# Kernel optimization log

Measured on AMD Instinct MI355X. Metric: run time of the kernel, lower is better.

## Reference

```python
import jax, jax.numpy as jnp
import numpy as np

B, T, C, E, K = 8, 2048, 1024, 8, 2
CAP = int(T / E * 1.25)  # expert capacity per batch row = 320


def setup_inputs() -> dict:
    key = jax.random.key(0)
    ks = jax.random.split(key, 6)
    s = lambda k, shape, fan: jax.random.normal(k, shape, jnp.float32) / np.sqrt(fan)
    return dict(
        x=jax.random.normal(ks[0], (B, T, C), jnp.float32),
        rw1=s(ks[1], (C, 4 * C), C), rb1=jnp.zeros((4 * C,), jnp.float32),
        rw2=s(ks[2], (4 * C, 4 * C), 4 * C), rb2=jnp.zeros((4 * C,), jnp.float32),
        rw3=s(ks[3], (4 * C, E), 4 * C), rb3=jnp.zeros((E,), jnp.float32),
        ew1=s(ks[4], (E, C, 4 * C), C), eb1=jnp.zeros((E, 4 * C), jnp.float32),
        ew2=s(ks[5], (E, 4 * C, C), 4 * C), eb2=jnp.zeros((E, C), jnp.float32),
    )


def reference(x, rw1, rb1, rw2, rb2, rw3, rb3, ew1, eb1, ew2, eb2):
    # Router (dropout is identity in eval): MLP -> softmax over experts
    h = jax.nn.relu(x @ rw1 + rb1)
    h = jax.nn.relu(h @ rw2 + rb2)
    probs = jax.nn.softmax(h @ rw3 + rb3, axis=-1)        # [B,T,E]
    topk_p, topk_e = jax.lax.top_k(probs, K)              # [B,T,K]

    b_ids = jnp.broadcast_to(jnp.arange(B)[:, None], (B, T))
    out = jnp.zeros_like(x)
    # Loop over small fixed number of experts (mirrors per-rank expert compute)
    for e in range(E):
        sel = (topk_e == e)                               # [B,T,K]
        mask = sel.any(-1)                                # token routed to expert e
        gate = (topk_p * sel).sum(-1)                     # unnormalized top-k prob
        pos = jnp.cumsum(mask, axis=1) - 1                # slot within capacity buffer
        keep = mask & (pos < CAP)                         # capacity truncation (drop overflow)
        pos_s = jnp.where(keep, pos, CAP)                 # CAP is out-of-range -> dropped
        # Dispatch: scatter kept tokens into [B, CAP, C] capacity-padded buffer
        buf = jnp.zeros((B, CAP, C), x.dtype).at[b_ids, pos_s].set(x, mode='drop')
        # Expert FFN on padded buffer
        y = jax.nn.relu(buf @ ew1[e] + eb1[e]) @ ew2[e] + eb2[e]
        # Combine: gather back to token positions, weight by gate
        g = y[b_ids, jnp.where(keep, pos, 0)]
        out = out + gate[..., None] * jnp.where(keep[..., None], g, jnp.zeros((), x.dtype))
    return out
```

## Files before the change

kernel.cpp:

```cpp
#include <hip/hip_runtime.h>
#include <stdint.h>

typedef _Float16 f16;
typedef _Float16 half8 __attribute__((ext_vector_type(8)));
typedef float f32x4 __attribute__((ext_vector_type(4)));

#define NF_MAX 2048
#define THETA  0.02f

__device__ __forceinline__ void gload16(const void* g, void* l) {
  __builtin_amdgcn_global_load_lds(
      (const __attribute__((address_space(1))) void*)g,
      (__attribute__((address_space(3))) void*)l, 16, 0, 0);
}

#define BAR() do { __builtin_amdgcn_s_barrier(); __builtin_amdgcn_sched_barrier(0); } while (0)
#define WAIT_VM8() do { asm volatile("s_waitcnt vmcnt(8)" ::: "memory"); __builtin_amdgcn_sched_barrier(0); } while (0)
#define WAIT_VM0() do { asm volatile("s_waitcnt vmcnt(0)" ::: "memory"); __builtin_amdgcn_sched_barrier(0); } while (0)

template<int EPI, bool SPLIT3>
__launch_bounds__(512, 2)
__global__ void gemm256(const f16* __restrict__ A0, const f16* __restrict__ A1,
                        const f16* __restrict__ B0, const f16* __restrict__ B1,
                        int N, int Kd, int lda, int ldb,
                        const int* __restrict__ rowsrcA, const f16* __restrict__ zeroPage,
                        const float* __restrict__ bias, int bias_stride, int rows_per_exp,
                        f16* __restrict__ oH, int ldo, float* __restrict__ oAcc,
                        const float* __restrict__ w3, float* __restrict__ oLog,
                        const int* __restrict__ nfp)
{
  __shared__ f16 lds[4 * 8192 * 2 + 512];
  f16* sA = lds;
  f16* sB = lds + 4 * 8192;
  f16* sDummy = lds + 8 * 8192;

  const int tid  = threadIdx.x;
  const int lane = tid & 63, w = tid >> 6;
  const int wm = w >> 2, wn = w & 3;

  const int gx  = gridDim.x;
  const int nwg = gx * gridDim.y;
  const int bid = blockIdx.y * gx + blockIdx.x;
  const int swz = (bid & 7) * (nwg >> 3) + (bid >> 3);
  const int by  = swz / gx, bx = swz - by * gx;
  const int m0  = by * 256, n0 = bx * 256;
  const int k0  = blockIdx.z * Kd;

  if (nfp) {
    int nf = *nfp; nf = nf < NF_MAX ? nf : NF_MAX;
    const int lim = (nf + 255) & ~255;
    if (m0 >= lim) return;
  }

  int e = 0;
  if (rows_per_exp > 0) e = m0 / rows_per_exp;
  const f16* Bh = B0 + (size_t)e * N * ldb;

  const int nk  = Kd >> 6;
  const int NIT = SPLIT3 ? 3 * nk : nk;

  const int sr  = lane & 15;
  const int sk8 = lane >> 4;

  size_t aoff[2], boff[2];
  bool az[2] = { false, false };
  #pragma unroll
  for (int jj = 0; jj < 2; ++jj) {
    const int arow = m0 + (jj * 8 + w) * 16 + sr;
    if (rowsrcA) {
      const int rs = rowsrcA[arow];
      az[jj] = (rs < 0);
      aoff[jj] = az[jj] ? 0 : (size_t)rs * lda;
    } else {
      aoff[jj] = (size_t)arow * lda;
    }
    boff[jj] = (size_t)(n0 + (jj * 8 + w) * 16 + sr) * ldb;
  }

  auto stageA = [&](const f16* base, int kk, int kc, f16* slotBase, bool valid) {
    #pragma unroll
    for (int jj = 0; jj < 2; ++jj) {
      const int mt = jj * 8 + w;
      f16* dst = valid ? (slotBase + mt * 512) : sDummy;
      const f16* src = az[jj] ? zeroPage
                              : base + aoff[jj] + (k0 + kk + kc * 32 + sk8 * 8);
      gload16(src, dst);
    }
  };
  auto stageB = [&](const f16* base, int kk, int kc, f16* slotBase, bool valid) {
    #pragma unroll
    for (int jj = 0; jj < 2; ++jj) {
      const int mt = jj * 8 + w;
      f16* dst = valid ? (slotBase + mt * 512) : sDummy;
      const f16* src = base + boff[jj] + (k0 + kk + kc * 32 + sk8 * 8);
      gload16(src, dst);
    }
  };

  struct It { const f16* Ab; const f16* Bb; int kk, kin, pass; };
  const f16* Ab0 = SPLIT3 ? A1 : A0;
  auto advance = [&](It& s) {
    if (s.kin + 1 < nk) { s.kin++; }
    else if (SPLIT3 && s.pass < 2) {
      s.kin = 0; s.pass++;
      s.Ab = (s.pass == 0) ? A1 : A0;
      s.Bb = (s.pass == 1) ? B1 : Bh;
    }
    s.kk = s.kin << 6;
  };
  It it1 = { Ab0, Bh, 64, 1, 0 };
  It it2 = { Ab0, Bh, 128, 2, 0 };

  stageA(Ab0, 0, 0, &sA[0], true);
  stageB(Bh,  0, 0, &sB[0], true);
  stageA(Ab0, 0, 1, &sA[8192], true);
  stageB(Bh,  0, 1, &sB[8192], true);
  stageA(it1.Ab, it1.kk, 0, &sA[2 * 8192], true);
  stageB(it1.Bb, it1.kk, 0, &sB[2 * 8192], true);
  WAIT_VM8();
  BAR();

  f32x4 acc[8][4] = {};
  const int aBase = wm * 8;
  const int bBase = wn * 4;

  auto mfma32 = [&](half8* a8, half8* bf) {
    __builtin_amdgcn_s_setprio(1);
    #pragma unroll
    for (int mi = 0; mi < 8; ++mi)
      #pragma unroll
      for (int ni = 0; ni < 4; ++ni)
        acc[mi][ni] = __builtin_amdgcn_mfma_f32_16x16x32_f16(
            a8[mi], bf[ni], acc[mi][ni], 0, 0, 0);
    __builtin_amdgcn_s_setprio(0);
  };
  auto rdA = [&](half8* dst, int slot, int mtb) {
    #pragma unroll
    for (int mi = 0; mi < 4; ++mi)
      dst[mi] = *(const half8*)&sA[slot * 8192 + (mtb + mi) * 512 + lane * 8];
  };
  auto rdB = [&](half8* dst, int slot) {
    #pragma unroll
    for (int ni = 0; ni < 4; ++ni)
      dst[ni] = *(const half8*)&sB[slot * 8192 + (bBase + ni) * 512 + lane * 8];
  };

  for (int t = 0; t < NIT; ++t) {
    const int sa0 = (2 * t) & 3, sa1 = sa0 ^ 1;
    const bool v1 = (t + 1 < NIT), v2 = (t + 2 < NIT);

    if (SPLIT3 && t == 2 * nk) {
      #pragma unroll
      for (int mi = 0; mi < 8; ++mi)
        #pragma unroll
        for (int ni = 0; ni < 4; ++ni)
          acc[mi][ni] = acc[mi][ni] * 2.44140625e-4f;
    }

    half8 a8[8], bF[4];

    rdA(&a8[0], sa0, aBase);
    rdA(&a8[4], sa0, aBase + 4);
    rdB(bF, sa0);
    stageA(it1.Ab, it1.kk, 1, &sA[(sa0 ^ 3) * 8192], v1);
    stageB(it1.Bb, it1.kk, 1, &sB[(sa0 ^ 3) * 8192], v1);
    WAIT_VM8();
    BAR();
    mfma32(a8, bF);
    BAR();

    rdA(&a8[0], sa1, aBase);
    rdA(&a8[4], sa1, aBase + 4);
    rdB(bF, sa1);
    stageA(it2.Ab, it2.kk, 0, &sA[sa0 * 8192], v2);
    stageB(it2.Bb, it2.kk, 0, &sB[sa0 * 8192], v2);
    WAIT_VM8();
    BAR();
    mfma32(a8, bF);
    BAR();

    it1 = it2;
    advance(it2);
  }
  WAIT_VM0();

  float bv[4] = { 0.f, 0.f, 0.f, 0.f };
  if (bias) {
    #pragma unroll
    for (int ni = 0; ni < 4; ++ni) {
      const int col = n0 + wn * 64 + ni * 16 + (lane & 15);
      bv[ni] = bias[(size_t)e * bias_stride + col];
    }
  }

  if (EPI == 2) {
    f32x4 wlo[4], whi[4];
    #pragma unroll
    for (int ni = 0; ni < 4; ++ni) {
      const int col = n0 + wn * 64 + ni * 16 + (lane & 15);
      wlo[ni] = *(const f32x4*)(w3 + (size_t)col * 8);
      whi[ni] = *(const f32x4*)(w3 + (size_t)col * 8 + 4);
    }
    const int p = (n0 >> 8) * 4 + wn;
    #pragma unroll
    for (int mi = 0; mi < 8; ++mi) {
      #pragma unroll
      for (int r = 0; r < 4; ++r) {
        const int row = m0 + wm * 128 + mi * 16 + (lane >> 4) * 4 + r;
        f32x4 plo = {}, phi = {};
        #pragma unroll
        for (int ni = 0; ni < 4; ++ni) {
          const float v = fmaxf(acc[mi][ni][r] + bv[ni], 0.f);
          plo += v * wlo[ni];
          phi += v * whi[ni];
        }
        #pragma unroll
        for (int msk = 1; msk < 16; msk <<= 1) {
          #pragma unroll
          for (int q = 0; q < 4; ++q) {
            plo[q] += __shfl_xor(plo[q], msk);
            phi[q] += __shfl_xor(phi[q], msk);
          }
        }
        if ((lane & 15) == 0) {
          float* dst = oLog + ((size_t)p * ldo + row) * 8;
          *(f32x4*)dst = plo;
          *(f32x4*)(dst + 4) = phi;
        }
      }
    }
  } else {
    #pragma unroll
    for (int mi = 0; mi < 8; ++mi) {
      #pragma unroll
      for (int r = 0; r < 4; ++r) {
        const int row = m0 + wm * 128 + mi * 16 + (lane >> 4) * 4 + r;
        #pragma unroll
        for (int ni = 0; ni < 4; ++ni) {
          const int col = n0 + wn * 64 + ni * 16 + (lane & 15);
          if (EPI == 3) {
            atomicAdd(&oAcc[(size_t)row * ldo + col], acc[mi][ni][r]);
          } else {
            float v = acc[mi][ni][r] + bv[ni];
            if (EPI == 0) v = fmaxf(v, 0.f);
            oH[(size_t)row * ldo + col] = (f16)v;
          }
        }
      }
    }
  }
}

__global__ void split_x(const float* __restrict__ x, f16* __restrict__ hi,
                        f16* __restrict__ lo, int n)
{
  const int i = blockIdx.x * 256 + threadIdx.x;
  if (i * 8 >= n) return;
  const f32x4 a = ((const f32x4*)x)[2 * i];
  const f32x4 b = ((const f32x4*)x)[2 * i + 1];
  half8 h, l;
  #pragma unroll
  for (int j = 0; j < 4; ++j) {
    float v = a[j]; f16 hh = (f16)v;
    h[j] = hh; l[j] = (f16)((v - (float)hh) * 4096.0f);
    v = b[j]; hh = (f16)v;
    h[4 + j] = hh; l[4 + j] = (f16)((v - (float)hh) * 4096.0f);
  }
  ((half8*)hi)[i] = h;
  ((half8*)lo)[i] = l;
}

template<bool SPLIT>
__global__ void transpose_conv(const float* __restrict__ in, f16* __restrict__ oh,
                               f16* __restrict__ ol, int R, int Cc)
{
  __shared__ float tile[64][65];
  const size_t boff = (size_t)blockIdx.z * R * Cc;
  in += boff; oh += boff;
  if (SPLIT) ol += boff;
  const int c0 = blockIdx.x * 64, r0 = blockIdx.y * 64;
  #pragma unroll
  for (int i = 0; i < 16; ++i) {
    const int idx = i * 256 + threadIdx.x;
    const int r = idx >> 6, c = idx & 63;
    tile[r][c] = in[(size_t)(r0 + r) * Cc + (c0 + c)];
  }
  __syncthreads();
  #pragma unroll
  for (int i = 0; i < 16; ++i) {
    const int idx = i * 256 + threadIdx.x;
    const int ro = idx >> 6, co = idx & 63;
    const float v = tile[co][ro];
    const f16 h = (f16)v;
    const size_t o = (size_t)(c0 + ro) * R + (r0 + co);
    oh[o] = h;
    if (SPLIT) ol[o] = (f16)((v - (float)h) * 4096.0f);
  }
}

__global__ void topk_flag(const float* __restrict__ part, const float* __restrict__ b3,
                          int* __restrict__ eidx, float* __restrict__ gval,
                          int* __restrict__ flags, int* __restrict__ nfc)
{
  const int t = blockIdx.x * 256 + threadIdx.x;
  float l[8];
  #pragma unroll
  for (int e = 0; e < 8; ++e) l[e] = b3[e];
  for (int p = 0; p < 64; ++p) {
    const float* src = part + ((size_t)p * 16384 + t) * 8;
    const f32x4 a = *(const f32x4*)src;
    const f32x4 b = *(const f32x4*)(src + 4);
    #pragma unroll
    for (int q = 0; q < 4; ++q) { l[q] += a[q]; l[4 + q] += b[q]; }
  }
  float mx = l[0];
  #pragma unroll
  for (int e = 1; e < 8; ++e) mx = fmaxf(mx, l[e]);
  float ex[8], s = 0.f;
  #pragma unroll
  for (int e = 0; e < 8; ++e) { ex[e] = expf(l[e] - mx); s += ex[e]; }
  float p1 = -1.f, p2 = -1.f; int e1 = 0, e2 = 0;
  #pragma unroll
  for (int e = 0; e < 8; ++e) {
    const float pe = ex[e] / s;
    if (pe > p1)      { p2 = p1; e2 = e1; p1 = pe; e1 = e; }
    else if (pe > p2) { p2 = pe; e2 = e; }
  }
  eidx[t * 2] = e1; eidx[t * 2 + 1] = e2;
  gval[t * 2] = p1; gval[t * 2 + 1] = p2;
  float l1 = -1e30f, l2 = -1e30f, l3 = -1e30f;
  #pragma unroll
  for (int e = 0; e < 8; ++e) {
    const float le = l[e];
    if (le > l1)      { l3 = l2; l2 = l1; l1 = le; }
    else if (le > l2) { l3 = l2; l2 = le; }
    else if (le > l3) { l3 = le; }
  }
  if (l2 - l3 < THETA) {
    const int s0 = atomicAdd(nfc, 1);
    if (s0 < NF_MAX) flags[s0] = t;
  }
}

__global__ void post1(const float* __restrict__ h1r, const float* __restrict__ b1,
                      f16* __restrict__ hh, f16* __restrict__ hl,
                      const int* __restrict__ nfc)
{
  int nf = *nfc; nf = nf < NF_MAX ? nf : NF_MAX;
  const int lim = (nf + 255) & ~255;
  const int row = blockIdx.x;
  if (row >= lim) return;
  const int j = blockIdx.y * 2048 + threadIdx.x * 8;
  const float* src = h1r + (size_t)row * 4096 + j;
  const f32x4 a = *(const f32x4*)src;
  const f32x4 b = *(const f32x4*)(src + 4);
  half8 h, l;
  #pragma unroll
  for (int k = 0; k < 4; ++k) {
    float v = fmaxf(a[k] + b1[j + k], 0.f);
    f16 x = (f16)v; h[k] = x; l[k] = (f16)((v - (float)x) * 4096.0f);
    v = fmaxf(b[k] + b1[j + 4 + k], 0.f);
    x = (f16)v; h[4 + k] = x; l[4 + k] = (f16)((v - (float)x) * 4096.0f);
  }
  *(half8*)(hh + (size_t)row * 4096 + j) = h;
  *(half8*)(hl + (size_t)row * 4096 + j) = l;
}

__global__ void logits_exact(const float* __restrict__ h2r, const float* __restrict__ b2,
                             const float* __restrict__ w3, const float* __restrict__ b3,
                             const int* __restrict__ flags, const int* __restrict__ nfc,
                             int* __restrict__ eidx, float* __restrict__ gval)
{
  const int srow = blockIdx.x;
  int nf = *nfc; nf = nf < NF_MAX ? nf : NF_MAX;
  if (srow >= nf) return;
  const float* hrow = h2r + (size_t)srow * 4096;
  double p[8];
  #pragma unroll
  for (int e = 0; e < 8; ++e) p[e] = 0.0;
  for (int i = 0; i < 16; ++i) {
    const int k = i * 256 + threadIdx.x;
    const double h = (double)fmaxf(hrow[k] + b2[k], 0.f);
    const float* wp = w3 + (size_t)k * 8;
    #pragma unroll
    for (int e = 0; e < 8; ++e) p[e] += h * (double)wp[e];
  }
  #pragma unroll
  for (int e = 0; e < 8; ++e)
    for (int off = 32; off > 0; off >>= 1)
      p[e] += __shfl_down(p[e], off);
  __shared__ double sp[4][8];
  const int lane = threadIdx.x & 63, wv = threadIdx.x >> 6;
  if (lane == 0) {
    #pragma unroll
    for (int e = 0; e < 8; ++e) sp[wv][e] = p[e];
  }
  __syncthreads();
  if (threadIdx.x == 0) {
    float l[8];
    #pragma unroll
    for (int e = 0; e < 8; ++e)
      l[e] = (float)(sp[0][e] + sp[1][e] + sp[2][e] + sp[3][e] + (double)b3[e]);
    float mx = l[0];
    for (int e = 1; e < 8; ++e) mx = fmaxf(mx, l[e]);
    float ex[8], s = 0.f;
    for (int e = 0; e < 8; ++e) { ex[e] = expf(l[e] - mx); s += ex[e]; }
    float p1 = -1.f, p2 = -1.f; int e1 = 0, e2 = 0;
    for (int e = 0; e < 8; ++e) {
      const float pe = ex[e] / s;
      if (pe > p1)      { p2 = p1; e2 = e1; p1 = pe; e1 = e; }
      else if (pe > p2) { p2 = pe; e2 = e; }
    }
    const int tok = flags[srow];
    eidx[tok * 2] = e1; eidx[tok * 2 + 1] = e2;
    gval[tok * 2] = p1; gval[tok * 2 + 1] = p2;
  }
}

__global__ void route_scan(const int* __restrict__ eidx, const float* __restrict__ gval,
                           int* __restrict__ cnt, int* __restrict__ rowsrc,
                           int* __restrict__ tokslot)
{
  const int pair = blockIdx.x;
  const int e = pair >> 3, b = pair & 7;
  const int lane = threadIdx.x;
  int running = 0;
  for (int t0 = 0; t0 < 2048; t0 += 64) {
    const int t = t0 + lane;
    const int i2 = (b * 2048 + t) * 2;
    const int m0 = (eidx[i2] == e), m1 = (eidx[i2 + 1] == e);
    const int m = m0 | m1;
    const unsigned long long bal = __ballot(m);
    const int pos = running + __popcll(bal & ((1ull << lane) - 1ull));
    if (m && pos < 320) {
      const int slot = pair * 320 + pos;
      rowsrc[slot] = b * 2048 + t;
      tokslot[(b * 2048 + t) * 2 + (m0 ? 0 : 1)] = slot;
    }
    running += __popcll(bal);
  }
  const int c = running < 320 ? running : 320;
  for (int s = c + lane; s < 320; s += 64) rowsrc[pair * 320 + s] = -1;
  if (lane == 0) cnt[pair] = c;
}

__global__ void combine(const f16* __restrict__ yb, const int* __restrict__ tokslot,
                        const float* __restrict__ gval, float* __restrict__ out)
{
  const int t = blockIdx.x;
  const int s0 = tokslot[t * 2], s1 = tokslot[t * 2 + 1];
  const float g0 = gval[t * 2], g1 = gval[t * 2 + 1];
  float a[8] = {};
  if (s0 >= 0) {
    const half8 y = ((const half8*)(yb + (size_t)s0 * 1024))[threadIdx.x];
    #pragma unroll
    for (int k = 0; k < 8; ++k) a[k] += g0 * (float)y[k];
  }
  if (s1 >= 0) {
    const half8 y = ((const half8*)(yb + (size_t)s1 * 1024))[threadIdx.x];
    #pragma unroll
    for (int k = 0; k < 8; ++k) a[k] += g1 * (float)y[k];
  }
  float* dst = out + (size_t)t * 1024 + threadIdx.x * 8;
  f32x4 lo = { a[0], a[1], a[2], a[3] }, hi = { a[4], a[5], a[6], a[7] };
  *(f32x4*)dst = lo;
  *(f32x4*)(dst + 4) = hi;
}

extern "C" void kernel_launch(void* const* d_in, const int* in_sizes, int n_in,
                              void* d_out, int out_size, void* d_ws, size_t ws_size,
                              hipStream_t stream)
{
  (void)in_sizes; (void)n_in; (void)out_size;
  const float* x   = (const float*)d_in[0];
  const float* rw1 = (const float*)d_in[1];
  const float* rb1 = (const float*)d_in[2];
  const float* rw2 = (const float*)d_in[3];
  const float* rb2 = (const float*)d_in[4];
  const float* rw3 = (const float*)d_in[5];
  const float* rb3 = (const float*)d_in[6];
  const float* ew1 = (const float*)d_in[7];
  const float* eb1 = (const float*)d_in[8];
  const float* ew2 = (const float*)d_in[9];
  const float* eb2 = (const float*)d_in[10];

  constexpr size_t MB = 1024ull * 1024ull;
  constexpr size_t KB = 1024ull;
  char* ws = (char*)d_ws;
  if (ws_size < 401 * MB) return;

  f16*   h1f  = (f16*)(ws);
  f16*   ew1t = (f16*)(ws);
  f16*   ew2t = (f16*)(ws + 64 * MB);
  f16*   xhi  = (f16*)(ws + 128 * MB);
  char*  S    = ws + 160 * MB;
  int*   eidx   = (int*)(S);
  float* gval   = (float*)(S + 128 * KB);
  int*   cnt    = (int*)(S + 256 * KB);
  int*   nfc    = (int*)(S + 260 * KB);
  int*   flags  = (int*)(S + 264 * KB);
  int*   tokslot= (int*)(S + 272 * KB);
  int*   rowsrc = (int*)(S + 400 * KB);
  f16*   zeros  = (f16*)(S + 480 * KB);
  f16*   xlo    = (f16*)(ws + 161 * MB);
  f16*   rw1thi = (f16*)(ws + 193 * MB);
  f16*   rw1tlo = (f16*)(ws + 201 * MB);
  f16*   rw2thi = (f16*)(ws + 209 * MB);
  f16*   rw2tlo = (f16*)(ws + 241 * MB);
  float* part   = (float*)(ws + 273 * MB);
  float* h1r    = (float*)(ws + 305 * MB);
  float* h2r    = (float*)(ws + 337 * MB);
  f16*   h1rh   = (f16*)(ws + 369 * MB);
  f16*   h1rl   = (f16*)(ws + 385 * MB);
  f16*   h_e    = (f16*)(ws + 161 * MB);
  f16*   yb     = (f16*)(ws + 321 * MB);

  hipMemsetAsync(nfc, 0, 4, stream);
  hipMemsetAsync(tokslot, 0xFF, 128 * KB, stream);
  hipMemsetAsync(zeros, 0, 16 * KB, stream);
  hipMemsetAsync(h1r, 0, 64 * MB, stream);

  split_x<<<8192, 256, 0, stream>>>(x, xhi, xlo, 16384 * 1024);
  transpose_conv<true ><<<dim3(64, 16, 1), 256, 0, stream>>>(rw1, rw1thi, rw1tlo, 1024, 4096);
  transpose_conv<true ><<<dim3(64, 64, 1), 256, 0, stream>>>(rw2, rw2thi, rw2tlo, 4096, 4096);

  gemm256<0, false><<<dim3(16, 64), 512, 0, stream>>>(
      xhi, nullptr, rw1thi, nullptr, 4096, 1024, 1024, 1024,
      nullptr, nullptr, rb1, 0, 0,
      h1f, 4096, nullptr, nullptr, nullptr, nullptr);
  gemm256<2, false><<<dim3(16, 64), 512, 0, stream>>>(
      h1f, nullptr, rw2thi, nullptr, 4096, 4096, 4096, 4096,
      nullptr, nullptr, rb2, 0, 0,
      nullptr, 16384, nullptr, rw3, part, nullptr);
  topk_flag<<<64, 256, 0, stream>>>(part, rb3, eidx, gval, flags, nfc);

  gemm256<3, true><<<dim3(16, 8, 2), 512, 0, stream>>>(
      xhi, xlo, rw1thi, rw1tlo, 4096, 512, 1024, 1024,
      flags, zeros, nullptr, 0, 0,
      nullptr, 4096, h1r, nullptr, nullptr, nfc);
  post1<<<dim3(2048, 2), 256, 0, stream>>>(h1r, rb1, h1rh, h1rl, nfc);
  gemm256<3, true><<<dim3(16, 8, 4), 512, 0, stream>>>(
      h1rh, h1rl, rw2thi, rw2tlo, 4096, 1024, 4096, 4096,
      nullptr, nullptr, nullptr, 0, 0,
      nullptr, 4096, h2r, nullptr, nullptr, nfc);
  logits_exact<<<NF_MAX, 256, 0, stream>>>(h2r, rb2, rw3, rb3, flags, nfc,
                                           eidx, gval);

  route_scan<<<64, 64, 0, stream>>>(eidx, gval, cnt, rowsrc, tokslot);

  transpose_conv<false><<<dim3(64, 16, 8), 256, 0, stream>>>(ew1, ew1t, nullptr, 1024, 4096);
  transpose_conv<false><<<dim3(16, 64, 8), 256, 0, stream>>>(ew2, ew2t, nullptr, 4096, 1024);

  gemm256<0, false><<<dim3(16, 80), 512, 0, stream>>>(
      xhi, nullptr, ew1t, nullptr, 4096, 1024, 1024, 1024,
      rowsrc, zeros, eb1, 4096, 2560,
      h_e, 4096, nullptr, nullptr, nullptr, nullptr);
  gemm256<1, false><<<dim3(4, 80), 512, 0, stream>>>(
      h_e, nullptr, ew2t, nullptr, 1024, 4096, 4096, 4096,
      nullptr, nullptr, eb2, 1024, 2560,
      yb, 1024, nullptr, nullptr, nullptr, nullptr);

  combine<<<16384, 128, 0, stream>>>(yb, tokslot, gval, (float*)d_out);
}
```

Before: 1.821 ms.

## Replace pipelined 256x256 GEMM with simpler single-buffered 128x128 tile GEMM

Swaps the 512-thread, 256x256-tile GEMM, which used a multi-slot LDS ring with vmcnt-based prefetch, for a 256-thread 128x128-tile kernel. The new kernel loads one K=32 chunk per iteration and brackets it with __syncthreads. The aim is more workgroups, higher occupancy and less LDS and register pressure per block. In exchange it loses the global-to-LDS prefetch overlap and halves per-tile data reuse, so the GEMMs may become more latency- and bandwidth-bound.

```diff
diff --git a/kernel.cpp b/kernel.cpp
--- a/kernel.cpp
+++ b/kernel.cpp
@@ -14,13 +14,9 @@
       (__attribute__((address_space(3))) void*)l, 16, 0, 0);
 }
 
-#define BAR() do { __builtin_amdgcn_s_barrier(); __builtin_amdgcn_sched_barrier(0); } while (0)
-#define WAIT_VM8() do { asm volatile("s_waitcnt vmcnt(8)" ::: "memory"); __builtin_amdgcn_sched_barrier(0); } while (0)
-#define WAIT_VM0() do { asm volatile("s_waitcnt vmcnt(0)" ::: "memory"); __builtin_amdgcn_sched_barrier(0); } while (0)
-
 template<int EPI, bool SPLIT3>
-__launch_bounds__(512, 2)
-__global__ void gemm256(const f16* __restrict__ A0, const f16* __restrict__ A1,
+__launch_bounds__(256, 4)
+__global__ void gemm128(const f16* __restrict__ A0, const f16* __restrict__ A1,
                         const f16* __restrict__ B0, const f16* __restrict__ B1,
                         int N, int Kd, int lda, int ldb,
                         const int* __restrict__ rowsrcA, const f16* __restrict__ zeroPage,
@@ -29,26 +25,23 @@
                         const float* __restrict__ w3, float* __restrict__ oLog,
                         const int* __restrict__ nfp)
 {
-  __shared__ f16 lds[4 * 8192 * 2 + 512];
-  f16* sA = lds;
-  f16* sB = lds + 4 * 8192;
-  f16* sDummy = lds + 8 * 8192;
-
-  const int tid  = threadIdx.x;
-  const int lane = tid & 63, w = tid >> 6;
-  const int wm = w >> 2, wn = w & 3;
+  __shared__ f16 sA[4096];
+  __shared__ f16 sB[4096];
+
+  const int lane = threadIdx.x & 63, w = threadIdx.x >> 6;
+  const int wm = w >> 1, wn = w & 1;
 
   const int gx  = gridDim.x;
   const int nwg = gx * gridDim.y;
   const int bid = blockIdx.y * gx + blockIdx.x;
   const int swz = (bid & 7) * (nwg >> 3) + (bid >> 3);
   const int by  = swz / gx, bx = swz - by * gx;
-  const int m0  = by * 256, n0 = bx * 256;
+  const int m0  = by * 128, n0 = bx * 128;
   const int k0  = blockIdx.z * Kd;
 
   if (nfp) {
     int nf = *nfp; nf = nf < NF_MAX ? nf : NF_MAX;
-    const int lim = (nf + 255) & ~255;
+    const int lim = (nf + 127) & ~127;
     if (m0 >= lim) return;
   }
 
@@ -56,7 +49,7 @@
   if (rows_per_exp > 0) e = m0 / rows_per_exp;
   const f16* Bh = B0 + (size_t)e * N * ldb;
 
-  const int nk  = Kd >> 6;
+  const int nk  = Kd >> 5;
   const int NIT = SPLIT3 ? 3 * nk : nk;
 
   const int sr  = lane & 15;
@@ -66,7 +59,7 @@
   bool az[2] = { false, false };
   #pragma unroll
   for (int jj = 0; jj < 2; ++jj) {
-    const int arow = m0 + (jj * 8 + w) * 16 + sr;
+    const int arow = m0 + (jj * 4 + w) * 16 + sr;
     if (rowsrcA) {
       const int rs = rowsrcA[arow];
       az[jj] = (rs < 0);
@@ -74,115 +67,53 @@
     } else {
       aoff[jj] = (size_t)arow * lda;
     }
-    boff[jj] = (size_t)(n0 + (jj * 8 + w) * 16 + sr) * ldb;
-  }
-
-  auto stageA = [&](const f16* base, int kk, int kc, f16* slotBase, bool valid) {
+    boff[jj] = (size_t)(n0 + (jj * 4 + w) * 16 + sr) * ldb;
+  }
+
+  f32x4 acc[4][4] = {};
+  int kin = 0, pass = 0;
+
+  for (int t = 0; t < NIT; ++t) {
+    const f16* Ab;
+    const f16* Bb;
+    if (SPLIT3) {
+      if (t == 2 * nk) {
+        #pragma unroll
+        for (int mi = 0; mi < 4; ++mi)
+          #pragma unroll
+          for (int ni = 0; ni < 4; ++ni)
+            acc[mi][ni] = acc[mi][ni] * 2.44140625e-4f;
+      }
+      Ab = (pass == 0) ? A1 : A0;
+      Bb = (pass == 1) ? B1 : Bh;
+    } else { Ab = A0; Bb = Bh; }
+    const int kk = k0 + (kin << 5) + sk8 * 8;
+
     #pragma unroll
     for (int jj = 0; jj < 2; ++jj) {
-      const int mt = jj * 8 + w;
-      f16* dst = valid ? (slotBase + mt * 512) : sDummy;
-      const f16* src = az[jj] ? zeroPage
-                              : base + aoff[jj] + (k0 + kk + kc * 32 + sk8 * 8);
-      gload16(src, dst);
-    }
-  };
-  auto stageB = [&](const f16* base, int kk, int kc, f16* slotBase, bool valid) {
-    #pragma unroll
-    for (int jj = 0; jj < 2; ++jj) {
-      const int mt = jj * 8 + w;
-      f16* dst = valid ? (slotBase + mt * 512) : sDummy;
-      const f16* src = base + boff[jj] + (k0 + kk + kc * 32 + sk8 * 8);
-      gload16(src, dst);
-    }
-  };
-
-  struct It { const f16* Ab; const f16* Bb; int kk, kin, pass; };
-  const f16* Ab0 = SPLIT3 ? A1 : A0;
-  auto advance = [&](It& s) {
-    if (s.kin + 1 < nk) { s.kin++; }
-    else if (SPLIT3 && s.pass < 2) {
-      s.kin = 0; s.pass++;
-      s.Ab = (s.pass == 0) ? A1 : A0;
-      s.Bb = (s.pass == 1) ? B1 : Bh;
-    }
-    s.kk = s.kin << 6;
-  };
-  It it1 = { Ab0, Bh, 64, 1, 0 };
-  It it2 = { Ab0, Bh, 128, 2, 0 };
-
-  stageA(Ab0, 0, 0, &sA[0], true);
-  stageB(Bh,  0, 0, &sB[0], true);
-  stageA(Ab0, 0, 1, &sA[8192], true);
-  stageB(Bh,  0, 1, &sB[8192], true);
-  stageA(it1.Ab, it1.kk, 0, &sA[2 * 8192], true);
-  stageB(it1.Bb, it1.kk, 0, &sB[2 * 8192], true);
-  WAIT_VM8();
-  BAR();
-
-  f32x4 acc[8][4] = {};
-  const int aBase = wm * 8;
-  const int bBase = wn * 4;
-
-  auto mfma32 = [&](half8* a8, half8* bf) {
-    __builtin_amdgcn_s_setprio(1);
-    #pragma unroll
-    for (int mi = 0; mi < 8; ++mi)
+      const int ch = jj * 4 + w;
+      gload16(az[jj] ? zeroPage : (Ab + aoff[jj] + kk), (void*)&sA[ch * 512]);
+      gload16(Bb + boff[jj] + kk,                       (void*)&sB[ch * 512]);
+    }
+    __syncthreads();
+
+    half8 aF[4], bF[4];
+    #pragma unroll
+    for (int mi = 0; mi < 4; ++mi)
+      aF[mi] = *(const half8*)&sA[(wm * 4 + mi) * 512 + lane * 8];
+    #pragma unroll
+    for (int ni = 0; ni < 4; ++ni)
+      bF[ni] = *(const half8*)&sB[(wn * 4 + ni) * 512 + lane * 8];
+    #pragma unroll
+    for (int mi = 0; mi < 4; ++mi)
       #pragma unroll
       for (int ni = 0; ni < 4; ++ni)
         acc[mi][ni] = __builtin_amdgcn_mfma_f32_16x16x32_f16(
-            a8[mi], bf[ni], acc[mi][ni], 0, 0, 0);
-    __builtin_amdgcn_s_setprio(0);
-  };
-  auto rdA = [&](half8* dst, int slot, int mtb) {
-    #pragma unroll
-    for (int mi = 0; mi < 4; ++mi)
-      dst[mi] = *(const half8*)&sA[slot * 8192 + (mtb + mi) * 512 + lane * 8];
-  };
-  auto rdB = [&](half8* dst, int slot) {
-    #pragma unroll
-    for (int ni = 0; ni < 4; ++ni)
-      dst[ni] = *(const half8*)&sB[slot * 8192 + (bBase + ni) * 512 + lane * 8];
-  };
-
-  for (int t = 0; t < NIT; ++t) {
-    const int sa0 = (2 * t) & 3, sa1 = sa0 ^ 1;
-    const bool v1 = (t + 1 < NIT), v2 = (t + 2 < NIT);
-
-    if (SPLIT3 && t == 2 * nk) {
-      #pragma unroll
-      for (int mi = 0; mi < 8; ++mi)
-        #pragma unroll
-        for (int ni = 0; ni < 4; ++ni)
-          acc[mi][ni] = acc[mi][ni] * 2.44140625e-4f;
-    }
-
-    half8 a8[8], bF[4];
-
-    rdA(&a8[0], sa0, aBase);
-    rdA(&a8[4], sa0, aBase + 4);
-    rdB(bF, sa0);
-    stageA(it1.Ab, it1.kk, 1, &sA[(sa0 ^ 3) * 8192], v1);
-    stageB(it1.Bb, it1.kk, 1, &sB[(sa0 ^ 3) * 8192], v1);
-    WAIT_VM8();
-    BAR();
-    mfma32(a8, bF);
-    BAR();
-
-    rdA(&a8[0], sa1, aBase);
-    rdA(&a8[4], sa1, aBase + 4);
-    rdB(bF, sa1);
-    stageA(it2.Ab, it2.kk, 0, &sA[sa0 * 8192], v2);
-    stageB(it2.Bb, it2.kk, 0, &sB[sa0 * 8192], v2);
-    WAIT_VM8();
-    BAR();
-    mfma32(a8, bF);
-    BAR();
-
-    it1 = it2;
-    advance(it2);
-  }
-  WAIT_VM0();
+            aF[mi], bF[ni], acc[mi][ni], 0, 0, 0);
+    __syncthreads();
+
+    if (++kin == nk) { kin = 0; ++pass; }
+  }
 
   float bv[4] = { 0.f, 0.f, 0.f, 0.f };
   if (bias) {
@@ -201,12 +132,12 @@
       wlo[ni] = *(const f32x4*)(w3 + (size_t)col * 8);
       whi[ni] = *(const f32x4*)(w3 + (size_t)col * 8 + 4);
     }
-    const int p = (n0 >> 8) * 4 + wn;
-    #pragma unroll
-    for (int mi = 0; mi < 8; ++mi) {
+    const int p = (n0 >> 7) * 2 + wn;
+    #pragma unroll
+    for (int mi = 0; mi < 4; ++mi) {
       #pragma unroll
       for (int r = 0; r < 4; ++r) {
-        const int row = m0 + wm * 128 + mi * 16 + (lane >> 4) * 4 + r;
+        const int row = m0 + wm * 64 + mi * 16 + (lane >> 4) * 4 + r;
         f32x4 plo = {}, phi = {};
         #pragma unroll
         for (int ni = 0; ni < 4; ++ni) {
@@ -231,10 +162,10 @@
     }
   } else {
     #pragma unroll
-    for (int mi = 0; mi < 8; ++mi) {
+    for (int mi = 0; mi < 4; ++mi) {
       #pragma unroll
       for (int r = 0; r < 4; ++r) {
-        const int row = m0 + wm * 128 + mi * 16 + (lane >> 4) * 4 + r;
+        const int row = m0 + wm * 64 + mi * 16 + (lane >> 4) * 4 + r;
         #pragma unroll
         for (int ni = 0; ni < 4; ++ni) {
           const int col = n0 + wn * 64 + ni * 16 + (lane & 15);
@@ -524,22 +455,22 @@
   transpose_conv<true ><<<dim3(64, 16, 1), 256, 0, stream>>>(rw1, rw1thi, rw1tlo, 1024, 4096);
   transpose_conv<true ><<<dim3(64, 64, 1), 256, 0, stream>>>(rw2, rw2thi, rw2tlo, 4096, 4096);
 
-  gemm256<0, false><<<dim3(16, 64), 512, 0, stream>>>(
+  gemm128<0, false><<<dim3(32, 128), 256, 0, stream>>>(
       xhi, nullptr, rw1thi, nullptr, 4096, 1024, 1024, 1024,
       nullptr, nullptr, rb1, 0, 0,
       h1f, 4096, nullptr, nullptr, nullptr, nullptr);
-  gemm256<2, false><<<dim3(16, 64), 512, 0, stream>>>(
+  gemm128<2, false><<<dim3(32, 128), 256, 0, stream>>>(
       h1f, nullptr, rw2thi, nullptr, 4096, 4096, 4096, 4096,
       nullptr, nullptr, rb2, 0, 0,
       nullptr, 16384, nullptr, rw3, part, nullptr);
   topk_flag<<<64, 256, 0, stream>>>(part, rb3, eidx, gval, flags, nfc);
 
-  gemm256<3, true><<<dim3(16, 8, 2), 512, 0, stream>>>(
+  gemm128<3, true><<<dim3(32, 16, 2), 256, 0, stream>>>(
       xhi, xlo, rw1thi, rw1tlo, 4096, 512, 1024, 1024,
       flags, zeros, nullptr, 0, 0,
       nullptr, 4096, h1r, nullptr, nullptr, nfc);
   post1<<<dim3(2048, 2), 256, 0, stream>>>(h1r, rb1, h1rh, h1rl, nfc);
-  gemm256<3, true><<<dim3(16, 8, 4), 512, 0, stream>>>(
+  gemm128<3, true><<<dim3(32, 16, 4), 256, 0, stream>>>(
       h1rh, h1rl, rw2thi, rw2tlo, 4096, 1024, 4096, 4096,
       nullptr, nullptr, nullptr, 0, 0,
       nullptr, 4096, h2r, nullptr, nullptr, nfc);
@@ -551,11 +482,11 @@
   transpose_conv<false><<<dim3(64, 16, 8), 256, 0, stream>>>(ew1, ew1t, nullptr, 1024, 4096);
   transpose_conv<false><<<dim3(16, 64, 8), 256, 0, stream>>>(ew2, ew2t, nullptr, 4096, 1024);
 
-  gemm256<0, false><<<dim3(16, 80), 512, 0, stream>>>(
+  gemm128<0, false><<<dim3(32, 160), 256, 0, stream>>>(
       xhi, nullptr, ew1t, nullptr, 4096, 1024, 1024, 1024,
       rowsrc, zeros, eb1, 4096, 2560,
       h_e, 4096, nullptr, nullptr, nullptr, nullptr);
-  gemm256<1, false><<<dim3(4, 80), 512, 0, stream>>>(
+  gemm128<1, false><<<dim3(8, 160), 256, 0, stream>>>(
       h_e, nullptr, ew2t, nullptr, 1024, 4096, 4096, 4096,
       nullptr, nullptr, eb2, 1024, 2560,
       yb, 1024, nullptr, nullptr, nullptr, nullptr);
```

After: 2.596 ms. +42.5%, slower.
